# Kernel tuning notes

Hardware: AMD Instinct MI355X
Metric: run time of the kernel (lower is better)

The kernel has to match this reference:

```python
import jax, jax.numpy as jnp
import numpy as np


def setup_inputs() -> dict:
    key = jax.random.key(0)
    k1, k2, k3 = jax.random.split(key, 3)
    B, E, L, D = 32, 256, 2048, 256
    doc_state = jax.random.normal(k1, (B, L, D), dtype=jnp.float32)
    entity_mapping = jax.random.uniform(k2, (B, E, L), dtype=jnp.float32)
    entity_lens = jax.random.uniform(k3, (B, E), dtype=jnp.float32)
    return {"doc_state": doc_state, "entity_mapping": entity_mapping, "entity_lens": entity_lens}


def reference(doc_state, entity_mapping, entity_lens):
    # Original: (entity_mapping[:, :, :, None] * doc_state[:, None, :, :]).sum(2) / entity_lens[:, :, None]
    # This is a batched contraction over L; express as einsum to avoid the
    # huge [B, E, L, D] intermediate.
    summed = jnp.einsum('bel,bld->bed', entity_mapping, doc_state)  # [B, E, D]
    return summed / entity_lens[:, :, None]
```

## Files before the change

### kernel.cpp

```cpp
#include <hip/hip_runtime.h>
#include <stdint.h>

#define B_ 32
#define E_ 256
#define L_ 2048
#define D_ 256

#define BE 64
#define BD 128
#define BK 32
#define KS 4
#define KCHUNK (L_ / KS)
#define NKT (KCHUNK / BK)

typedef __attribute__((ext_vector_type(4))) float  f32x4;
typedef __attribute__((ext_vector_type(4))) short  s16x4;
typedef __attribute__((ext_vector_type(8))) short  s16x8;

__device__ __forceinline__ void cvt_hilo1(float x, short &h, short &l) {
    unsigned u = __builtin_bit_cast(unsigned, x);
    h = (short)(u >> 16);
    float hf = __builtin_bit_cast(float, u & 0xFFFF0000u);
    unsigned r = __builtin_bit_cast(unsigned, x - hf);
    l = (short)(r >> 16);
}

__global__ void zero_out_kernel(f32x4* __restrict__ out) {
    out[(size_t)blockIdx.x * 256 + threadIdx.x] = f32x4{0.f, 0.f, 0.f, 0.f};
}

__global__ __launch_bounds__(512, 8)
void mean_pool_kernel(const float* __restrict__ doc,
                      const float* __restrict__ emap,
                      const float* __restrict__ lens,
                      float* __restrict__ out) {
    __shared__ __align__(16) short As_hi[BE][BK];
    __shared__ __align__(16) short As_lo[BE][BK];
    __shared__ __align__(16) short Bs_hi[BD][BK];
    __shared__ __align__(16) short Bs_lo[BD][BK];
    __shared__ float lens_s[BE];

    const int t   = threadIdx.x;
    const int blk = blockIdx.x;
    const int ks  = blk & 3;
    const int d0  = ((blk >> 2) & 1) * BD;
    const int e0  = ((blk >> 3) & 3) * BE;
    const int b   = blk >> 5;

    const float* Ag = emap + ((size_t)b * E_ + e0) * L_ + ks * KCHUNK;
    const float* Sg = doc  + (size_t)b * L_ * D_ + (size_t)ks * KCHUNK * D_ + d0;

    if (t < BE) lens_s[t] = lens[b * E_ + e0 + t];

    const int a_c4 = t & 7;
    const int a_r  = t >> 3;
    const int b_d  = t & 127;
    const int b_g  = t >> 7;

    const int lane = t & 63;
    const int w    = t >> 6;
    const int eo   = (w & 1) * 32;
    const int dq   = (w >> 1) * 32;
    const int ml   = lane & 15;
    const int kg   = lane >> 4;

    f32x4 acc[2][2] = {};
    f32x4 pa;
    float pb[8];

    pa = *(const f32x4*)(Ag + (size_t)a_r * L_ + a_c4 * 4);
    #pragma unroll
    for (int j = 0; j < 8; ++j)
        pb[j] = Sg[(size_t)(b_g * 8 + j) * D_ + b_d];

    for (int kt = 0; kt < NKT; ++kt) {
        {
            s16x4 h, l;
            #pragma unroll
            for (int i = 0; i < 4; ++i) { short hh, ll; cvt_hilo1(pa[i], hh, ll); h[i] = hh; l[i] = ll; }
            const int col = (((a_c4 >> 1) ^ (a_r & 3)) << 3) + (a_c4 & 1) * 4;
            *(s16x4*)&As_hi[a_r][col] = h;
            *(s16x4*)&As_lo[a_r][col] = l;
        }
        {
            s16x8 h, l;
            #pragma unroll
            for (int j = 0; j < 8; ++j) {
                short hh, ll; cvt_hilo1(pb[j], hh, ll);
                h[j] = hh; l[j] = ll;
            }
            const int col = (b_g ^ ((b_d >> 1) & 3)) << 3;
            *(s16x8*)&Bs_hi[b_d][col] = h;
            *(s16x8*)&Bs_lo[b_d][col] = l;
        }
        __syncthreads();

        if (kt + 1 < NKT) {
            const int k0 = (kt + 1) * BK;
            pa = *(const f32x4*)(Ag + (size_t)a_r * L_ + k0 + a_c4 * 4);
            #pragma unroll
            for (int j = 0; j < 8; ++j)
                pb[j] = Sg[(size_t)(k0 + b_g * 8 + j) * D_ + b_d];
        }

        {
            s16x8 ah[2], al[2], bh[2], bl[2];
            #pragma unroll
            for (int mi = 0; mi < 2; ++mi) {
                const int row = eo + mi * 16 + ml;
                const int col = (kg ^ (row & 3)) << 3;
                ah[mi] = *(const s16x8*)&As_hi[row][col];
                al[mi] = *(const s16x8*)&As_lo[row][col];
            }
            #pragma unroll
            for (int ni = 0; ni < 2; ++ni) {
                const int row = dq + ni * 16 + ml;
                const int col = (kg ^ ((row >> 1) & 3)) << 3;
                bh[ni] = *(const s16x8*)&Bs_hi[row][col];
                bl[ni] = *(const s16x8*)&Bs_lo[row][col];
            }
            #pragma unroll
            for (int mi = 0; mi < 2; ++mi)
                #pragma unroll
                for (int ni = 0; ni < 2; ++ni) {
                    acc[mi][ni] = __builtin_amdgcn_mfma_f32_16x16x32_bf16(ah[mi], bh[ni], acc[mi][ni], 0, 0, 0);
                    acc[mi][ni] = __builtin_amdgcn_mfma_f32_16x16x32_bf16(ah[mi], bl[ni], acc[mi][ni], 0, 0, 0);
                    acc[mi][ni] = __builtin_amdgcn_mfma_f32_16x16x32_bf16(al[mi], bh[ni], acc[mi][ni], 0, 0, 0);
                }
        }
        __syncthreads();
    }

    #pragma unroll
    for (int mi = 0; mi < 2; ++mi) {
        #pragma unroll
        for (int rr = 0; rr < 4; ++rr) {
            const int er = eo + mi * 16 + kg * 4 + rr;
            const float lv = lens_s[er];
            #pragma unroll
            for (int ni = 0; ni < 2; ++ni) {
                atomicAdd(&out[((size_t)(b * E_ + e0 + er)) * D_ + d0 + dq + ni * 16 + ml],
                          acc[mi][ni][rr] / lv);
            }
        }
    }
}

extern "C" void kernel_launch(void* const* d_in, const int* in_sizes, int n_in,
                              void* d_out, int out_size, void* d_ws, size_t ws_size,
                              hipStream_t stream) {
    const float* doc  = (const float*)d_in[0];
    const float* emap = (const float*)d_in[1];
    const float* lens = (const float*)d_in[2];
    float* out = (float*)d_out;

    zero_out_kernel<<<dim3(out_size / (4 * 256)), dim3(256), 0, stream>>>((f32x4*)out);

    dim3 grid(B_ * (E_ / BE) * (D_ / BD) * KS);
    dim3 block(512);
    hipLaunchKernelGGL(mean_pool_kernel, grid, block, 0, stream,
                       doc, emap, lens, out);
}
```

Before: 176.1 us.

## Double-buffer LDS tiles with two-deep register prefetch and one barrier per step

Shared-memory A/B tiles are double-buffered and global loads are prefetched two K-steps ahead into registers. Each iteration now has a single LDS barrier instead of two, and the bf16 hi/lo split and store of the next tile overlaps with the MFMA work on the current tile. The aim is to hide global and LDS latency and cut synchronization. In exchange it doubles LDS use and raises register pressure, and the occupancy hint drops from 8 to 6.

```diff
diff --git a/kernel.cpp b/kernel.cpp
--- a/kernel.cpp
+++ b/kernel.cpp
@@ -25,19 +25,23 @@
     l = (short)(r >> 16);
 }
 
+__device__ __forceinline__ void lds_barrier() {
+    asm volatile("s_waitcnt lgkmcnt(0)\n\ts_barrier" ::: "memory");
+}
+
 __global__ void zero_out_kernel(f32x4* __restrict__ out) {
     out[(size_t)blockIdx.x * 256 + threadIdx.x] = f32x4{0.f, 0.f, 0.f, 0.f};
 }
 
-__global__ __launch_bounds__(512, 8)
+__global__ __launch_bounds__(512, 6)
 void mean_pool_kernel(const float* __restrict__ doc,
                       const float* __restrict__ emap,
                       const float* __restrict__ lens,
                       float* __restrict__ out) {
-    __shared__ __align__(16) short As_hi[BE][BK];
-    __shared__ __align__(16) short As_lo[BE][BK];
-    __shared__ __align__(16) short Bs_hi[BD][BK];
-    __shared__ __align__(16) short Bs_lo[BD][BK];
+    __shared__ __align__(16) short As_hi[2][BE][BK];
+    __shared__ __align__(16) short As_lo[2][BE][BK];
+    __shared__ __align__(16) short Bs_hi[2][BD][BK];
+    __shared__ __align__(16) short Bs_lo[2][BD][BK];
     __shared__ float lens_s[BE];
 
     const int t   = threadIdx.x;
@@ -65,70 +69,84 @@
     const int kg   = lane >> 4;
 
     f32x4 acc[2][2] = {};
-    f32x4 pa;
-    float pb[8];
+    f32x4 pa[2];
+    float pb[2][8];
 
-    pa = *(const f32x4*)(Ag + (size_t)a_r * L_ + a_c4 * 4);
     #pragma unroll
-    for (int j = 0; j < 8; ++j)
-        pb[j] = Sg[(size_t)(b_g * 8 + j) * D_ + b_d];
+    for (int s = 0; s < 2; ++s) {
+        const int k0 = s * BK;
+        pa[s] = *(const f32x4*)(Ag + (size_t)a_r * L_ + k0 + a_c4 * 4);
+        #pragma unroll
+        for (int j = 0; j < 8; ++j)
+            pb[s][j] = Sg[(size_t)(k0 + b_g * 8 + j) * D_ + b_d];
+    }
+    {
+        s16x4 h, l;
+        #pragma unroll
+        for (int i = 0; i < 4; ++i) { short hh, ll; cvt_hilo1(pa[0][i], hh, ll); h[i] = hh; l[i] = ll; }
+        const int col = (((a_c4 >> 1) ^ (a_r & 3)) << 3) + (a_c4 & 1) * 4;
+        *(s16x4*)&As_hi[0][a_r][col] = h;
+        *(s16x4*)&As_lo[0][a_r][col] = l;
+        s16x8 h8, l8;
+        #pragma unroll
+        for (int j = 0; j < 8; ++j) { short hh, ll; cvt_hilo1(pb[0][j], hh, ll); h8[j] = hh; l8[j] = ll; }
+        const int colb = (b_g ^ ((b_d >> 1) & 3)) << 3;
+        *(s16x8*)&Bs_hi[0][b_d][colb] = h8;
+        *(s16x8*)&Bs_lo[0][b_d][colb] = l8;
+    }
 
     for (int kt = 0; kt < NKT; ++kt) {
-        {
+        lds_barrier();
+        const int cur = kt & 1;
+
+        if (kt + 2 < NKT) {
+            const int k0 = (kt + 2) * BK;
+            pa[cur] = *(const f32x4*)(Ag + (size_t)a_r * L_ + k0 + a_c4 * 4);
+            #pragma unroll
+            for (int j = 0; j < 8; ++j)
+                pb[cur][j] = Sg[(size_t)(k0 + b_g * 8 + j) * D_ + b_d];
+        }
+
+        s16x8 ah[2], al[2], bh[2], bl[2];
+        #pragma unroll
+        for (int mi = 0; mi < 2; ++mi) {
+            const int row = eo + mi * 16 + ml;
+            const int col = (kg ^ (row & 3)) << 3;
+            ah[mi] = *(const s16x8*)&As_hi[cur][row][col];
+            al[mi] = *(const s16x8*)&As_lo[cur][row][col];
+        }
+        #pragma unroll
+        for (int ni = 0; ni < 2; ++ni) {
+            const int row = dq + ni * 16 + ml;
+            const int col = (kg ^ ((row >> 1) & 3)) << 3;
+            bh[ni] = *(const s16x8*)&Bs_hi[cur][row][col];
+            bl[ni] = *(const s16x8*)&Bs_lo[cur][row][col];
+        }
+
+        if (kt + 1 < NKT) {
+            const int nxt = cur ^ 1;
             s16x4 h, l;
             #pragma unroll
-            for (int i = 0; i < 4; ++i) { short hh, ll; cvt_hilo1(pa[i], hh, ll); h[i] = hh; l[i] = ll; }
+            for (int i = 0; i < 4; ++i) { short hh, ll; cvt_hilo1(pa[nxt][i], hh, ll); h[i] = hh; l[i] = ll; }
             const int col = (((a_c4 >> 1) ^ (a_r & 3)) << 3) + (a_c4 & 1) * 4;
-            *(s16x4*)&As_hi[a_r][col] = h;
-            *(s16x4*)&As_lo[a_r][col] = l;
-        }
-        {
-            s16x8 h, l;
+            *(s16x4*)&As_hi[nxt][a_r][col] = h;
+            *(s16x4*)&As_lo[nxt][a_r][col] = l;
+            s16x8 h8, l8;
             #pragma unroll
-            for (int j = 0; j < 8; ++j) {
-                short hh, ll; cvt_hilo1(pb[j], hh, ll);
-                h[j] = hh; l[j] = ll;
-            }
-            const int col = (b_g ^ ((b_d >> 1) & 3)) << 3;
-            *(s16x8*)&Bs_hi[b_d][col] = h;
-            *(s16x8*)&Bs_lo[b_d][col] = l;
-        }
-        __syncthreads();
-
-        if (kt + 1 < NKT) {
-            const int k0 = (kt + 1) * BK;
-            pa = *(const f32x4*)(Ag + (size_t)a_r * L_ + k0 + a_c4 * 4);
-            #pragma unroll
-            for (int j = 0; j < 8; ++j)
-                pb[j] = Sg[(size_t)(k0 + b_g * 8 + j) * D_ + b_d];
+            for (int j = 0; j < 8; ++j) { short hh, ll; cvt_hilo1(pb[nxt][j], hh, ll); h8[j] = hh; l8[j] = ll; }
+            const int colb = (b_g ^ ((b_d >> 1) & 3)) << 3;
+            *(s16x8*)&Bs_hi[nxt][b_d][colb] = h8;
+            *(s16x8*)&Bs_lo[nxt][b_d][colb] = l8;
         }
 
-        {
-            s16x8 ah[2], al[2], bh[2], bl[2];
-            #pragma unroll
-            for (int mi = 0; mi < 2; ++mi) {
-                const int row = eo + mi * 16 + ml;
-                const int col = (kg ^ (row & 3)) << 3;
-                ah[mi] = *(const s16x8*)&As_hi[row][col];
-                al[mi] = *(const s16x8*)&As_lo[row][col];
-            }
+        #pragma unroll
+        for (int mi = 0; mi < 2; ++mi)
             #pragma unroll
             for (int ni = 0; ni < 2; ++ni) {
-                const int row = dq + ni * 16 + ml;
-                const int col = (kg ^ ((row >> 1) & 3)) << 3;
-                bh[ni] = *(const s16x8*)&Bs_hi[row][col];
-                bl[ni] = *(const s16x8*)&Bs_lo[row][col];
+                acc[mi][ni] = __builtin_amdgcn_mfma_f32_16x16x32_bf16(ah[mi], bh[ni], acc[mi][ni], 0, 0, 0);
+                acc[mi][ni] = __builtin_amdgcn_mfma_f32_16x16x32_bf16(ah[mi], bl[ni], acc[mi][ni], 0, 0, 0);
+                acc[mi][ni] = __builtin_amdgcn_mfma_f32_16x16x32_bf16(al[mi], bh[ni], acc[mi][ni], 0, 0, 0);
             }
-            #pragma unroll
-            for (int mi = 0; mi < 2; ++mi)
-                #pragma unroll
-                for (int ni = 0; ni < 2; ++ni) {
-                    acc[mi][ni] = __builtin_amdgcn_mfma_f32_16x16x32_bf16(ah[mi], bh[ni], acc[mi][ni], 0, 0, 0);
-                    acc[mi][ni] = __builtin_amdgcn_mfma_f32_16x16x32_bf16(ah[mi], bl[ni], acc[mi][ni], 0, 0, 0);
-                    acc[mi][ni] = __builtin_amdgcn_mfma_f32_16x16x32_bf16(al[mi], bh[ni], acc[mi][ni], 0, 0, 0);
-                }
-        }
-        __syncthreads();
     }
 
     #pragma unroll
```

Measured after the change: 179.7 us. 1.02x slower.

## Drop LDS staging and load MFMA operands directly from global per wave

Applied to the files above, without the earlier changes.

Replaces the block-level shared-memory tiling with independent per-wave 32x64 output tiles whose operands are loaded straight from global memory into registers. Loads for the next k-step are double-buffered in registers, and the per-step __syncthreads barriers are gone. Blocks shrink to 256 threads and the grid is reorganised so each wave covers one (batch, e-tile, d-tile, k-split) slice. The cost is lost cross-wave reuse: emap and doc are fetched more times through cache, the hi/lo bf16 split is recomputed redundantly, and the doc loads become 64-byte strided scalar accesses.

```diff
diff --git a/kernel.cpp b/kernel.cpp
--- a/kernel.cpp
+++ b/kernel.cpp
@@ -5,16 +5,11 @@
 #define E_ 256
 #define L_ 2048
 #define D_ 256
-
-#define BE 64
-#define BD 128
-#define BK 32
 #define KS 4
 #define KCHUNK (L_ / KS)
-#define NKT (KCHUNK / BK)
+#define NKT (KCHUNK / 32)
 
 typedef __attribute__((ext_vector_type(4))) float  f32x4;
-typedef __attribute__((ext_vector_type(4))) short  s16x4;
 typedef __attribute__((ext_vector_type(8))) short  s16x8;
 
 __device__ __forceinline__ void cvt_hilo1(float x, short &h, short &l) {
@@ -29,121 +24,99 @@
     out[(size_t)blockIdx.x * 256 + threadIdx.x] = f32x4{0.f, 0.f, 0.f, 0.f};
 }
 
-__global__ __launch_bounds__(512, 8)
+__global__ __launch_bounds__(256, 3)
 void mean_pool_kernel(const float* __restrict__ doc,
                       const float* __restrict__ emap,
                       const float* __restrict__ lens,
                       float* __restrict__ out) {
-    __shared__ __align__(16) short As_hi[BE][BK];
-    __shared__ __align__(16) short As_lo[BE][BK];
-    __shared__ __align__(16) short Bs_hi[BD][BK];
-    __shared__ __align__(16) short Bs_lo[BD][BK];
-    __shared__ float lens_s[BE];
-
-    const int t   = threadIdx.x;
-    const int blk = blockIdx.x;
-    const int ks  = blk & 3;
-    const int d0  = ((blk >> 2) & 1) * BD;
-    const int e0  = ((blk >> 3) & 3) * BE;
-    const int b   = blk >> 5;
-
-    const float* Ag = emap + ((size_t)b * E_ + e0) * L_ + ks * KCHUNK;
-    const float* Sg = doc  + (size_t)b * L_ * D_ + (size_t)ks * KCHUNK * D_ + d0;
-
-    if (t < BE) lens_s[t] = lens[b * E_ + e0 + t];
-
-    const int a_c4 = t & 7;
-    const int a_r  = t >> 3;
-    const int b_d  = t & 127;
-    const int b_g  = t >> 7;
-
+    const int t    = threadIdx.x;
     const int lane = t & 63;
-    const int w    = t >> 6;
-    const int eo   = (w & 1) * 32;
-    const int dq   = (w >> 1) * 32;
+    const int gw   = blockIdx.x * 4 + (t >> 6);
+    const int ks   = gw & 3;
+    const int dt   = (gw >> 2) & 3;
+    const int e8   = (gw >> 4) & 7;
+    const int b    = gw >> 7;
+    const int d0   = dt * 64;
+    const int e0   = e8 * 32;
     const int ml   = lane & 15;
     const int kg   = lane >> 4;
 
-    f32x4 acc[2][2] = {};
-    f32x4 pa;
-    float pb[8];
+    const float* Ab = emap + ((size_t)(b * E_ + e0 + ml)) * L_ + ks * KCHUNK + kg * 8;
+    const float* Bb = doc  + ((size_t)(b * L_ + ks * KCHUNK + kg * 8)) * D_ + d0 + ml;
 
-    pa = *(const f32x4*)(Ag + (size_t)a_r * L_ + a_c4 * 4);
+    f32x4 av[2][2][2];
+    float bv[2][4][8];
+    f32x4 acc[2][4] = {};
+
     #pragma unroll
-    for (int j = 0; j < 8; ++j)
-        pb[j] = Sg[(size_t)(b_g * 8 + j) * D_ + b_d];
+    for (int mi = 0; mi < 2; ++mi) {
+        av[0][mi][0] = *(const f32x4*)(Ab + (size_t)mi * 16 * L_);
+        av[0][mi][1] = *(const f32x4*)(Ab + (size_t)mi * 16 * L_ + 4);
+    }
+    #pragma unroll
+    for (int ni = 0; ni < 4; ++ni)
+        #pragma unroll
+        for (int j = 0; j < 8; ++j)
+            bv[0][ni][j] = Bb[(size_t)j * D_ + ni * 16];
 
+    #pragma unroll 2
     for (int kt = 0; kt < NKT; ++kt) {
-        {
-            s16x4 h, l;
+        const int cur = kt & 1, nxt = cur ^ 1;
+
+        if (kt + 1 < NKT) {
+            const int kc = (kt + 1) * 32;
             #pragma unroll
-            for (int i = 0; i < 4; ++i) { short hh, ll; cvt_hilo1(pa[i], hh, ll); h[i] = hh; l[i] = ll; }
-            const int col = (((a_c4 >> 1) ^ (a_r & 3)) << 3) + (a_c4 & 1) * 4;
-            *(s16x4*)&As_hi[a_r][col] = h;
-            *(s16x4*)&As_lo[a_r][col] = l;
+            for (int mi = 0; mi < 2; ++mi) {
+                av[nxt][mi][0] = *(const f32x4*)(Ab + (size_t)mi * 16 * L_ + kc);
+                av[nxt][mi][1] = *(const f32x4*)(Ab + (size_t)mi * 16 * L_ + kc + 4);
+            }
+            #pragma unroll
+            for (int ni = 0; ni < 4; ++ni)
+                #pragma unroll
+                for (int j = 0; j < 8; ++j)
+                    bv[nxt][ni][j] = Bb[(size_t)(kc + j) * D_ + ni * 16];
         }
-        {
-            s16x8 h, l;
+
+        s16x8 ah[2], al[2];
+        #pragma unroll
+        for (int mi = 0; mi < 2; ++mi)
+            #pragma unroll
+            for (int ii = 0; ii < 8; ++ii) {
+                short hh, ll;
+                cvt_hilo1(av[cur][mi][ii >> 2][ii & 3], hh, ll);
+                ah[mi][ii] = hh; al[mi][ii] = ll;
+            }
+        s16x8 bh[4], bl[4];
+        #pragma unroll
+        for (int ni = 0; ni < 4; ++ni)
             #pragma unroll
             for (int j = 0; j < 8; ++j) {
-                short hh, ll; cvt_hilo1(pb[j], hh, ll);
-                h[j] = hh; l[j] = ll;
+                short hh, ll;
+                cvt_hilo1(bv[cur][ni][j], hh, ll);
+                bh[ni][j] = hh; bl[ni][j] = ll;
             }
-            const int col = (b_g ^ ((b_d >> 1) & 3)) << 3;
-            *(s16x8*)&Bs_hi[b_d][col] = h;
-            *(s16x8*)&Bs_lo[b_d][col] = l;
-        }
-        __syncthreads();
 
-        if (kt + 1 < NKT) {
-            const int k0 = (kt + 1) * BK;
-            pa = *(const f32x4*)(Ag + (size_t)a_r * L_ + k0 + a_c4 * 4);
+        #pragma unroll
+        for (int mi = 0; mi < 2; ++mi)
             #pragma unroll
-            for (int j = 0; j < 8; ++j)
-                pb[j] = Sg[(size_t)(k0 + b_g * 8 + j) * D_ + b_d];
-        }
-
-        {
-            s16x8 ah[2], al[2], bh[2], bl[2];
-            #pragma unroll
-            for (int mi = 0; mi < 2; ++mi) {
-                const int row = eo + mi * 16 + ml;
-                const int col = (kg ^ (row & 3)) << 3;
-                ah[mi] = *(const s16x8*)&As_hi[row][col];
-                al[mi] = *(const s16x8*)&As_lo[row][col];
+            for (int ni = 0; ni < 4; ++ni) {
+                acc[mi][ni] = __builtin_amdgcn_mfma_f32_16x16x32_bf16(ah[mi], bh[ni], acc[mi][ni], 0, 0, 0);
+                acc[mi][ni] = __builtin_amdgcn_mfma_f32_16x16x32_bf16(ah[mi], bl[ni], acc[mi][ni], 0, 0, 0);
+                acc[mi][ni] = __builtin_amdgcn_mfma_f32_16x16x32_bf16(al[mi], bh[ni], acc[mi][ni], 0, 0, 0);
             }
-            #pragma unroll
-            for (int ni = 0; ni < 2; ++ni) {
-                const int row = dq + ni * 16 + ml;
-                const int col = (kg ^ ((row >> 1) & 3)) << 3;
-                bh[ni] = *(const s16x8*)&Bs_hi[row][col];
-                bl[ni] = *(const s16x8*)&Bs_lo[row][col];
-            }
-            #pragma unroll
-            for (int mi = 0; mi < 2; ++mi)
-                #pragma unroll
-                for (int ni = 0; ni < 2; ++ni) {
-                    acc[mi][ni] = __builtin_amdgcn_mfma_f32_16x16x32_bf16(ah[mi], bh[ni], acc[mi][ni], 0, 0, 0);
-                    acc[mi][ni] = __builtin_amdgcn_mfma_f32_16x16x32_bf16(ah[mi], bl[ni], acc[mi][ni], 0, 0, 0);
-                    acc[mi][ni] = __builtin_amdgcn_mfma_f32_16x16x32_bf16(al[mi], bh[ni], acc[mi][ni], 0, 0, 0);
-                }
-        }
-        __syncthreads();
     }
 
     #pragma unroll
-    for (int mi = 0; mi < 2; ++mi) {
+    for (int mi = 0; mi < 2; ++mi)
         #pragma unroll
         for (int rr = 0; rr < 4; ++rr) {
-            const int er = eo + mi * 16 + kg * 4 + rr;
-            const float lv = lens_s[er];
+            const int er = e0 + mi * 16 + kg * 4 + rr;
+            const float lv = lens[b * E_ + er];
             #pragma unroll
-            for (int ni = 0; ni < 2; ++ni) {
-                atomicAdd(&out[((size_t)(b * E_ + e0 + er)) * D_ + d0 + dq + ni * 16 + ml],
+            for (int ni = 0; ni < 4; ++ni)
+                atomicAdd(&out[((size_t)(b * E_ + er)) * D_ + d0 + ni * 16 + ml],
                           acc[mi][ni][rr] / lv);
-            }
         }
-    }
 }
 
 extern "C" void kernel_launch(void* const* d_in, const int* in_sizes, int n_in,
@@ -156,8 +129,8 @@
 
     zero_out_kernel<<<dim3(out_size / (4 * 256)), dim3(256), 0, stream>>>((f32x4*)out);
 
-    dim3 grid(B_ * (E_ / BE) * (D_ / BD) * KS);
-    dim3 block(512);
+    dim3 grid(1024);
+    dim3 block(256);
     hipLaunchKernelGGL(mean_pool_kernel, grid, block, 0, stream,
                        doc, emap, lens, out);
 }
```

After: 206.9 us. +17.5%, slower.

## Enlarge per-wave register tile to 64x64 with 256-thread blocks

Applied to the files above, without the earlier changes.

The entity tile grows from 64 to 128 rows and the block shrinks from 512 to 256 threads. Each wave now computes a 64x64 output sub-tile with a 4x4 MFMA accumulator array instead of 2x2. This raises fragment reuse from shared memory and halves redundant global reads of doc_state across entity tiles. The costs are half as many blocks (512), higher register pressure and lower occupancy, which may expose more latency.

```diff
diff --git a/kernel.cpp b/kernel.cpp
--- a/kernel.cpp
+++ b/kernel.cpp
@@ -6,7 +6,7 @@
 #define L_ 2048
 #define D_ 256
 
-#define BE 64
+#define BE 128
 #define BD 128
 #define BK 32
 #define KS 4
@@ -29,7 +29,7 @@
     out[(size_t)blockIdx.x * 256 + threadIdx.x] = f32x4{0.f, 0.f, 0.f, 0.f};
 }
 
-__global__ __launch_bounds__(512, 8)
+__global__ __launch_bounds__(256, 2)
 void mean_pool_kernel(const float* __restrict__ doc,
                       const float* __restrict__ emap,
                       const float* __restrict__ lens,
@@ -44,8 +44,8 @@
     const int blk = blockIdx.x;
     const int ks  = blk & 3;
     const int d0  = ((blk >> 2) & 1) * BD;
-    const int e0  = ((blk >> 3) & 3) * BE;
-    const int b   = blk >> 5;
+    const int e0  = ((blk >> 3) & 1) * BE;
+    const int b   = blk >> 4;
 
     const float* Ag = emap + ((size_t)b * E_ + e0) * L_ + ks * KCHUNK;
     const float* Sg = doc  + (size_t)b * L_ * D_ + (size_t)ks * KCHUNK * D_ + d0;
@@ -55,41 +55,49 @@
     const int a_c4 = t & 7;
     const int a_r  = t >> 3;
     const int b_d  = t & 127;
-    const int b_g  = t >> 7;
+    const int b_g0 = t >> 7;
 
     const int lane = t & 63;
     const int w    = t >> 6;
-    const int eo   = (w & 1) * 32;
-    const int dq   = (w >> 1) * 32;
+    const int eo   = (w & 1) * 64;
+    const int dq   = (w >> 1) * 64;
     const int ml   = lane & 15;
     const int kg   = lane >> 4;
 
-    f32x4 acc[2][2] = {};
-    f32x4 pa;
-    float pb[8];
+    f32x4 acc[4][4] = {};
+    f32x4 pa[4];
+    float pb[2][8];
 
-    pa = *(const f32x4*)(Ag + (size_t)a_r * L_ + a_c4 * 4);
     #pragma unroll
-    for (int j = 0; j < 8; ++j)
-        pb[j] = Sg[(size_t)(b_g * 8 + j) * D_ + b_d];
+    for (int rr = 0; rr < 4; ++rr)
+        pa[rr] = *(const f32x4*)(Ag + (size_t)(a_r + rr * 32) * L_ + a_c4 * 4);
+    #pragma unroll
+    for (int rr = 0; rr < 2; ++rr)
+        #pragma unroll
+        for (int j = 0; j < 8; ++j)
+            pb[rr][j] = Sg[(size_t)((b_g0 + rr * 2) * 8 + j) * D_ + b_d];
 
     for (int kt = 0; kt < NKT; ++kt) {
-        {
+        #pragma unroll
+        for (int rr = 0; rr < 4; ++rr) {
+            const int row = a_r + rr * 32;
             s16x4 h, l;
             #pragma unroll
-            for (int i = 0; i < 4; ++i) { short hh, ll; cvt_hilo1(pa[i], hh, ll); h[i] = hh; l[i] = ll; }
-            const int col = (((a_c4 >> 1) ^ (a_r & 3)) << 3) + (a_c4 & 1) * 4;
-            *(s16x4*)&As_hi[a_r][col] = h;
-            *(s16x4*)&As_lo[a_r][col] = l;
+            for (int i = 0; i < 4; ++i) { short hh, ll; cvt_hilo1(pa[rr][i], hh, ll); h[i] = hh; l[i] = ll; }
+            const int col = (((a_c4 >> 1) ^ (row & 3)) << 3) + (a_c4 & 1) * 4;
+            *(s16x4*)&As_hi[row][col] = h;
+            *(s16x4*)&As_lo[row][col] = l;
         }
-        {
+        #pragma unroll
+        for (int rr = 0; rr < 2; ++rr) {
+            const int g = b_g0 + rr * 2;
             s16x8 h, l;
             #pragma unroll
             for (int j = 0; j < 8; ++j) {
-                short hh, ll; cvt_hilo1(pb[j], hh, ll);
+                short hh, ll; cvt_hilo1(pb[rr][j], hh, ll);
                 h[j] = hh; l[j] = ll;
             }
-            const int col = (b_g ^ ((b_d >> 1) & 3)) << 3;
+            const int col = (g ^ ((b_d >> 1) & 3)) << 3;
             *(s16x8*)&Bs_hi[b_d][col] = h;
             *(s16x8*)&Bs_lo[b_d][col] = l;
         }
@@ -97,32 +105,36 @@
 
         if (kt + 1 < NKT) {
             const int k0 = (kt + 1) * BK;
-            pa = *(const f32x4*)(Ag + (size_t)a_r * L_ + k0 + a_c4 * 4);
             #pragma unroll
-            for (int j = 0; j < 8; ++j)
-                pb[j] = Sg[(size_t)(k0 + b_g * 8 + j) * D_ + b_d];
+            for (int rr = 0; rr < 4; ++rr)
+                pa[rr] = *(const f32x4*)(Ag + (size_t)(a_r + rr * 32) * L_ + k0 + a_c4 * 4);
+            #pragma unroll
+            for (int rr = 0; rr < 2; ++rr)
+                #pragma unroll
+                for (int j = 0; j < 8; ++j)
+                    pb[rr][j] = Sg[(size_t)(k0 + (b_g0 + rr * 2) * 8 + j) * D_ + b_d];
         }
 
         {
-            s16x8 ah[2], al[2], bh[2], bl[2];
+            s16x8 ah[4], al[4], bh[4], bl[4];
             #pragma unroll
-            for (int mi = 0; mi < 2; ++mi) {
+            for (int mi = 0; mi < 4; ++mi) {
                 const int row = eo + mi * 16 + ml;
                 const int col = (kg ^ (row & 3)) << 3;
                 ah[mi] = *(const s16x8*)&As_hi[row][col];
                 al[mi] = *(const s16x8*)&As_lo[row][col];
             }
             #pragma unroll
-            for (int ni = 0; ni < 2; ++ni) {
+            for (int ni = 0; ni < 4; ++ni) {
                 const int row = dq + ni * 16 + ml;
                 const int col = (kg ^ ((row >> 1) & 3)) << 3;
                 bh[ni] = *(const s16x8*)&Bs_hi[row][col];
                 bl[ni] = *(const s16x8*)&Bs_lo[row][col];
             }
             #pragma unroll
-            for (int mi = 0; mi < 2; ++mi)
+            for (int mi = 0; mi < 4; ++mi)
                 #pragma unroll
-                for (int ni = 0; ni < 2; ++ni) {
+                for (int ni = 0; ni < 4; ++ni) {
                     acc[mi][ni] = __builtin_amdgcn_mfma_f32_16x16x32_bf16(ah[mi], bh[ni], acc[mi][ni], 0, 0, 0);
                     acc[mi][ni] = __builtin_amdgcn_mfma_f32_16x16x32_bf16(ah[mi], bl[ni], acc[mi][ni], 0, 0, 0);
                     acc[mi][ni] = __builtin_amdgcn_mfma_f32_16x16x32_bf16(al[mi], bh[ni], acc[mi][ni], 0, 0, 0);
@@ -132,13 +144,13 @@
     }
 
     #pragma unroll
-    for (int mi = 0; mi < 2; ++mi) {
+    for (int mi = 0; mi < 4; ++mi) {
         #pragma unroll
         for (int rr = 0; rr < 4; ++rr) {
             const int er = eo + mi * 16 + kg * 4 + rr;
             const float lv = lens_s[er];
             #pragma unroll
-            for (int ni = 0; ni < 2; ++ni) {
+            for (int ni = 0; ni < 4; ++ni) {
                 atomicAdd(&out[((size_t)(b * E_ + e0 + er)) * D_ + d0 + dq + ni * 16 + ml],
                           acc[mi][ni][rr] / lv);
             }
@@ -157,7 +169,7 @@
     zero_out_kernel<<<dim3(out_size / (4 * 256)), dim3(256), 0, stream>>>((f32x4*)out);
 
     dim3 grid(B_ * (E_ / BE) * (D_ / BD) * KS);
-    dim3 block(512);
+    dim3 block(256);
     hipLaunchKernelGGL(mean_pool_kernel, grid, block, 0, stream,
                        doc, emap, lens, out);
 }
```

Measured after the change: 173.7 us. Within noise of the previous version (-1.4%).
